# Performance work log

Measured on AMD Instinct MI355X. Metric: run time of the kernel, lower is better.

## Reference

```python
import jax, jax.numpy as jnp
import numpy as np
import math

L = 8192          # original_window (signal length)
WIN = 128         # config.small_window == n_features
STRIDE = 32       # config.small_stride
EMB = 128         # embedding_dim -> rnn2 hidden
HID = 2 * EMB     # rnn1 hidden
B = 256


def _window_starts(length, w, s):
    count = math.ceil((length - w) / s)
    starts = [i * s for i in range(count)]
    if count * s < length:
        starts.append(length - w)  # trailing window, mirrors torch code
    return np.asarray(starts, dtype=np.int32)


def sliding_window(x):
    starts = _window_starts(L, WIN, STRIDE)          # [T]
    idx = starts[:, None] + np.arange(WIN)[None, :]
    return x[:, idx]


def lstm(x, W_ih, W_hh, b_ih, b_hh):
    # x: [B, T, I]; torch gate order i, f, g, o. Returns (all h: [B,T,H], last h: [B,H])
    H = W_hh.shape[1]
    bsz = x.shape[0]
    xg = jnp.einsum('bti,gi->btg', x, W_ih) + b_ih + b_hh  # precompute input gates [B,T,4H]

    def step(carry, g):
        h, c = carry
        g = g + h @ W_hh.T
        i, f, gg, o = jnp.split(g, 4, axis=-1)
        i = jax.nn.sigmoid(i)
        f = jax.nn.sigmoid(f)
        gg = jnp.tanh(gg)
        o = jax.nn.sigmoid(o)
        c = f * c + i * gg
        h = o * jnp.tanh(c)
        return (h, c), h

    h0 = jnp.zeros((bsz, H), x.dtype)
    c0 = jnp.zeros((bsz, H), x.dtype)
    (h_n, _), hs = jax.lax.scan(step, (h0, c0), jnp.swapaxes(xg, 0, 1))
    return jnp.swapaxes(hs, 0, 1), h_n


def setup_inputs() -> dict:
    key = jax.random.key(0)
    ks = jax.random.split(key, 9)
    s1 = 1.0 / np.sqrt(HID)
    s2 = 1.0 / np.sqrt(EMB)
    return {
        'x': jax.random.normal(ks[0], (B, L), jnp.float32),
        'W_ih1': jax.random.uniform(ks[1], (4 * HID, WIN), jnp.float32, -s1, s1),
        'W_hh1': jax.random.uniform(ks[2], (4 * HID, HID), jnp.float32, -s1, s1),
        'b_ih1': jax.random.uniform(ks[3], (4 * HID,), jnp.float32, -s1, s1),
        'b_hh1': jax.random.uniform(ks[4], (4 * HID,), jnp.float32, -s1, s1),
        'W_ih2': jax.random.uniform(ks[5], (4 * EMB, HID), jnp.float32, -s2, s2),
        'W_hh2': jax.random.uniform(ks[6], (4 * EMB, EMB), jnp.float32, -s2, s2),
        'b_ih2': jax.random.uniform(ks[7], (4 * EMB,), jnp.float32, -s2, s2),
        'b_hh2': jax.random.uniform(ks[8], (4 * EMB,), jnp.float32, -s2, s2),
    }


def reference(x, W_ih1, W_hh1, b_ih1, b_hh1, W_ih2, W_hh2, b_ih2, b_hh2):
    xw = sliding_window(x)
    h1, _ = lstm(xw, W_ih1, W_hh1, b_ih1, b_hh1)  # [B, T, HID]
    _, h_n = lstm(h1, W_ih2, W_hh2, b_ih2, b_hh2)  # [B, EMB]
    return h_n.reshape((x.shape[0], EMB))
```

## Files before the change

### kernel.cpp

```cpp
#include <hip/hip_runtime.h>
#include <stdint.h>

#define L_SIG   8192
#define T_STEPS 253
#define H1      256
#define H2      128
#define NBATCH  256

typedef __attribute__((ext_vector_type(8))) short short8;
typedef __attribute__((ext_vector_type(4))) float f32x4;
typedef unsigned int uint32x4 __attribute__((ext_vector_type(4)));
typedef unsigned int uint32x2 __attribute__((ext_vector_type(2)));

__device__ __forceinline__ ushort f2bf(float f){
  uint32_t u = __builtin_bit_cast(uint32_t, f);
  u += 0x7FFFu + ((u >> 16) & 1u);
  return (ushort)(u >> 16);
}
__device__ __forceinline__ float bf2f(ushort h){
  uint32_t u = ((uint32_t)h) << 16;
  return __builtin_bit_cast(float, u);
}
__device__ __forceinline__ float sigm(float x){ return 1.0f / (1.0f + __expf(-x)); }
__device__ __forceinline__ float tanhfast(float x){ return 1.0f - 2.0f / (__expf(2.0f*x) + 1.0f); }
__device__ __forceinline__ int swz(int u){ return u ^ ((u >> 3) & 7); }
__device__ __forceinline__ void load_coh(uint32x4& r, const unsigned int* p){
  asm volatile("global_load_dwordx4 %0, %1, off sc0 sc1" : "=&v"(r) : "v"(p));
}

__global__ __launch_bounds__(256, 1)
void encoder_kernel(const float* __restrict__ x,
                    const float* __restrict__ Wih1, const float* __restrict__ Whh1,
                    const float* __restrict__ bih1, const float* __restrict__ bhh1,
                    const float* __restrict__ Wih2, const float* __restrict__ Whh2,
                    const float* __restrict__ bih2, const float* __restrict__ bhh2,
                    float* __restrict__ out,
                    unsigned int* sync_ws,
                    unsigned int* h1buf,
                    unsigned int* h2buf)
{
  __shared__ ushort sh_hi[16][520];
  __shared__ ushort sh_lo[16][520];
  __shared__ float  sC1[4][16][20];
  __shared__ float  sC2[2][2][16][20];

  const int tid  = threadIdx.x;
  const int lane = tid & 63;
  const int wv   = tid >> 6;
  const int bid  = blockIdx.x;
  const int grp = 2 * (bid & 7) + (bid >> 7);
  const int bi  = (bid & 127) >> 3;
  const int B0  = grp * 16;
  const int D1  = bi * 16;
  const int D2  = bi * 8;

  short8 B1h[12], B1l[12];
  short8 B2h[6],  B2l[6];
  {
    const int nn = lane & 15, p = lane >> 4;
    const int R1 = wv * 256 + D1 + nn;
    #pragma unroll
    for (int kk = 0; kk < 12; ++kk){
      short8 h8, l8;
      #pragma unroll
      for (int j = 0; j < 8; ++j){
        const int k = 32*kk + 8*p + j;
        const float v = (k < 128) ? Wih1[R1*128 + k] : Whh1[R1*256 + (k - 128)];
        const ushort hb = f2bf(v);
        h8[j] = (short)hb;
        l8[j] = (short)f2bf(v - bf2f(hb));
      }
      B1h[kk] = h8; B1l[kk] = l8;
    }
    const int tw = wv & 1, kh = wv >> 1;
    const int rr = tw*16 + nn;
    const int R2 = (rr >> 3) * 128 + D2 + (rr & 7);
    #pragma unroll
    for (int i = 0; i < 6; ++i){
      const int kk2 = 6*kh + i;
      short8 h8, l8;
      #pragma unroll
      for (int j = 0; j < 8; ++j){
        const int k = 32*kk2 + 8*p + j;
        const float v = (k < 256) ? Wih2[R2*256 + k] : Whh2[R2*128 + (k - 256)];
        const ushort hb = f2bf(v);
        h8[j] = (short)hb;
        l8[j] = (short)f2bf(v - bf2f(hb));
      }
      B2h[i] = h8; B2l[i] = l8;
    }
  }

  const int eb  = tid >> 4, ed  = tid & 15;
  const int eb2 = (tid & 127) >> 3, ed2 = tid & 7;
  float bs1[4], bs2[4];
  #pragma unroll
  for (int g = 0; g < 4; ++g){
    bs1[g] = bih1[g*256 + D1 + ed]  + bhh1[g*256 + D1 + ed];
    bs2[g] = bih2[g*128 + D2 + ed2] + bhh2[g*128 + D2 + ed2];
  }

  float c1 = 0.f, c2 = 0.f;
  unsigned int* slots = sync_ws + grp * 64;

  auto stageX = [&](int wn){
    const int bx = tid >> 4, cx = tid & 15;
    const float* xp = x + (size_t)(B0 + bx) * L_SIG + 32*wn + 8*cx;
    const float4 v0 = *(const float4*)xp;
    const float4 v1 = *(const float4*)(xp + 4);
    float f[8] = {v0.x, v0.y, v0.z, v0.w, v1.x, v1.y, v1.z, v1.w};
    union { ushort s[8]; uint32x4 v; } H, L;
    #pragma unroll
    for (int j = 0; j < 8; ++j){
      const ushort hb = f2bf(f[j]);
      H.s[j] = hb;
      L.s[j] = f2bf(f[j] - bf2f(hb));
    }
    const int u = swz(cx);
    *(uint32x4*)&sh_hi[bx][8*u] = H.v;
    *(uint32x4*)&sh_lo[bx][8*u] = L.v;
  };

  auto wrState = [&](uint32x4 q, int b, int us){
    union { ushort s[4]; uint32x2 v; } Hh, Ll;
    #pragma unroll
    for (int k = 0; k < 4; ++k){
      const unsigned int u = q[k];
      Hh.s[k] = (ushort)(u & 0xFFFFu);
      Ll.s[k] = (ushort)(u >> 16);
    }
    *(uint32x2*)&sh_hi[b][us] = Hh.v;
    *(uint32x2*)&sh_lo[b][us] = Ll.v;
  };

  auto stageState = [&](int n){
    const unsigned int* h1p = h1buf + (size_t)(n & 1)*(NBATCH*H1) + (size_t)B0*H1 + 4*tid;
    uint32x4 q0, q1, q2, q3, q4, q5;
    load_coh(q0, h1p);
    load_coh(q1, h1p + 1024);
    load_coh(q2, h1p + 2048);
    load_coh(q3, h1p + 3072);
    const bool h2v = (n >= 1);
    if (h2v){
      const unsigned int* h2p = h2buf + (size_t)((n-1) & 1)*(NBATCH*H2) + (size_t)B0*H2 + 4*tid;
      load_coh(q4, h2p);
      load_coh(q5, h2p + 1024);
    }
    asm volatile("s_waitcnt vmcnt(0)" ::: "memory");
    __builtin_amdgcn_sched_barrier(0);
    {
      const int t6 = tid & 63;
      const int us = 8*swz(16 + (t6 >> 1)) + 4*(t6 & 1);
      const int b0r = tid >> 6;
      wrState(q0, b0r + 0,  us);
      wrState(q1, b0r + 4,  us);
      wrState(q2, b0r + 8,  us);
      wrState(q3, b0r + 12, us);
    }
    {
      const int t5 = tid & 31;
      const int us = 8*swz(48 + (t5 >> 1)) + 4*(t5 & 1);
      const int b0r = tid >> 5;
      if (h2v){
        wrState(q4, b0r + 0, us);
        wrState(q5, b0r + 8, us);
      } else {
        uint32x2 z = {0, 0};
        *(uint32x2*)&sh_hi[b0r + 0][us] = z; *(uint32x2*)&sh_lo[b0r + 0][us] = z;
        *(uint32x2*)&sh_hi[b0r + 8][us] = z; *(uint32x2*)&sh_lo[b0r + 8][us] = z;
      }
    }
  };

  for (int i = tid; i < 16*384; i += 256){
    const int b = i / 384, c = 128 + (i % 384);
    const int us = 8*swz(c >> 3) + (c & 7);
    sh_hi[b][us] = 0; sh_lo[b][us] = 0;
  }
  stageX(0);
  __syncthreads();

  for (int n = 0; n <= T_STEPS; ++n){
    const int m = lane & 15, p = lane >> 4;
    if (n < T_STEPS){
      f32x4 hh = {0,0,0,0}, hl = {0,0,0,0}, lh = {0,0,0,0};
      #pragma unroll
      for (int kk = 0; kk < 12; ++kk){
        const int u = swz(4*kk + p);
        const short8 ah = *(const short8*)&sh_hi[m][8*u];
        const short8 al = *(const short8*)&sh_lo[m][8*u];
        hh = __builtin_amdgcn_mfma_f32_16x16x32_bf16(ah, B1h[kk], hh, 0, 0, 0);
        hl = __builtin_amdgcn_mfma_f32_16x16x32_bf16(ah, B1l[kk], hl, 0, 0, 0);
        lh = __builtin_amdgcn_mfma_f32_16x16x32_bf16(al, B1h[kk], lh, 0, 0, 0);
      }
      const f32x4 cs = hh + hl + lh;
      #pragma unroll
      for (int r = 0; r < 4; ++r) sC1[wv][4*p + r][m] = cs[r];
    }
    if (n >= 1){
      const int tw = wv & 1, kh = wv >> 1;
      f32x4 hh = {0,0,0,0}, hl = {0,0,0,0}, lh = {0,0,0,0};
      #pragma unroll
      for (int i = 0; i < 6; ++i){
        const int u = swz(16 + 4*(6*kh + i) + p);
        const short8 ah = *(const short8*)&sh_hi[m][8*u];
        const short8 al = *(const short8*)&sh_lo[m][8*u];
        hh = __builtin_amdgcn_mfma_f32_16x16x32_bf16(ah, B2h[i], hh, 0, 0, 0);
        hl = __builtin_amdgcn_mfma_f32_16x16x32_bf16(ah, B2l[i], hl, 0, 0, 0);
        lh = __builtin_amdgcn_mfma_f32_16x16x32_bf16(al, B2h[i], lh, 0, 0, 0);
      }
      const f32x4 cs = hh + hl + lh;
      #pragma unroll
      for (int r = 0; r < 4; ++r) sC2[tw][kh][4*p + r][m] = cs[r];
    }
    __syncthreads();

    if (n < T_STEPS){
      float gi = sC1[0][eb][ed] + bs1[0];
      float gf = sC1[1][eb][ed] + bs1[1];
      float gg = sC1[2][eb][ed] + bs1[2];
      float go = sC1[3][eb][ed] + bs1[3];
      c1 = sigm(gf)*c1 + sigm(gi)*tanhfast(gg);
      const float h = sigm(go)*tanhfast(c1);
      const ushort hb = f2bf(h);
      const ushort lb = f2bf(h - bf2f(hb));
      __hip_atomic_store(
          &h1buf[(size_t)(n & 1)*(NBATCH*H1) + (size_t)(B0 + eb)*H1 + D1 + ed],
          (uint32_t)hb | ((uint32_t)lb << 16),
          __ATOMIC_RELAXED, __HIP_MEMORY_SCOPE_AGENT);
    }
    if (n >= 1 && tid < 128){
      float gi = sC2[0][0][eb2][ed2]   + sC2[0][1][eb2][ed2]   + bs2[0];
      float gf = sC2[0][0][eb2][8+ed2] + sC2[0][1][eb2][8+ed2] + bs2[1];
      float gg = sC2[1][0][eb2][ed2]   + sC2[1][1][eb2][ed2]   + bs2[2];
      float go = sC2[1][0][eb2][8+ed2] + sC2[1][1][eb2][8+ed2] + bs2[3];
      c2 = sigm(gf)*c2 + sigm(gi)*tanhfast(gg);
      const float h = sigm(go)*tanhfast(c2);
      if (n == T_STEPS){
        out[(size_t)(B0 + eb2)*H2 + D2 + ed2] = h;
      } else {
        const ushort hb = f2bf(h);
        const ushort lb = f2bf(h - bf2f(hb));
        __hip_atomic_store(
            &h2buf[(size_t)((n-1) & 1)*(NBATCH*H2) + (size_t)(B0 + eb2)*H2 + D2 + ed2],
            (uint32_t)hb | ((uint32_t)lb << 16),
            __ATOMIC_RELAXED, __HIP_MEMORY_SCOPE_AGENT);
      }
    }

    if (n < T_STEPS){
      __syncthreads();
      if (tid == 0){
        __hip_atomic_store(&slots[bi], (unsigned int)(n + 1),
                           __ATOMIC_RELAXED, __HIP_MEMORY_SCOPE_AGENT);
      }
      if (n + 1 < T_STEPS) stageX(n + 1);
      if (wv == 0){
        const unsigned int tgt = (unsigned int)(n + 1);
        while (true){
          const unsigned int v = __hip_atomic_load(&slots[lane & 15],
                                                   __ATOMIC_RELAXED, __HIP_MEMORY_SCOPE_AGENT);
          if (__all(v >= tgt)) break;
          __builtin_amdgcn_s_sleep(1);
        }
      }
      __syncthreads();
      stageState(n);
      __syncthreads();
    }
  }
}

extern "C" void kernel_launch(void* const* d_in, const int* in_sizes, int n_in,
                              void* d_out, int out_size, void* d_ws, size_t ws_size,
                              hipStream_t stream)
{
  const float* x    = (const float*)d_in[0];
  const float* Wih1 = (const float*)d_in[1];
  const float* Whh1 = (const float*)d_in[2];
  const float* bih1 = (const float*)d_in[3];
  const float* bhh1 = (const float*)d_in[4];
  const float* Wih2 = (const float*)d_in[5];
  const float* Whh2 = (const float*)d_in[6];
  const float* bih2 = (const float*)d_in[7];
  const float* bhh2 = (const float*)d_in[8];

  uint8_t*      ws    = (uint8_t*)d_ws;
  unsigned int* syncp = (unsigned int*)ws;
  unsigned int* h1buf = (unsigned int*)(ws + 4096);
  unsigned int* h2buf = (unsigned int*)(ws + 4096 + 2*NBATCH*H1*4);

  hipMemsetAsync(syncp, 0, 4096, stream);
  encoder_kernel<<<dim3(256), dim3(256), 0, stream>>>(
      x, Wih1, Whh1, bih1, bhh1, Wih2, Whh2, bih2, bhh2,
      (float*)d_out, syncp, h1buf, h2buf);
}
```

Measured before the change: 759.7 us.

## Replace flag barrier with step-tagged state words and split K across waves

Each hidden-state word now carries its step counter in a 64-bit pair, so consumers poll the state data directly instead of a separate per-block slot array. This removes a block barrier, the flag store and the spin loop per step. The MFMA work is also reorganised so each wave takes a K-slice for all gates, with partial sums reduced through shared memory, and the hl/lh accumulators are merged. In exchange, each state read is twice as wide, every thread re-polls a dozen vector loads until all tags match, and the host memset is larger.

```diff
diff --git a/kernel.cpp b/kernel.cpp
--- a/kernel.cpp
+++ b/kernel.cpp
@@ -24,8 +24,11 @@
 __device__ __forceinline__ float sigm(float x){ return 1.0f / (1.0f + __expf(-x)); }
 __device__ __forceinline__ float tanhfast(float x){ return 1.0f - 2.0f / (__expf(2.0f*x) + 1.0f); }
 __device__ __forceinline__ int swz(int u){ return u ^ ((u >> 3) & 7); }
-__device__ __forceinline__ void load_coh(uint32x4& r, const unsigned int* p){
+__device__ __forceinline__ void load4(uint32x4& r, const unsigned int* p){
   asm volatile("global_load_dwordx4 %0, %1, off sc0 sc1" : "=&v"(r) : "v"(p));
+}
+__device__ __forceinline__ void store2_coh(unsigned int* p, uint32x2 v){
+  asm volatile("global_store_dwordx2 %0, %1, off sc0 sc1" :: "v"(p), "v"(v) : "memory");
 }
 
 __global__ __launch_bounds__(256, 1)
@@ -35,14 +38,13 @@
                     const float* __restrict__ Wih2, const float* __restrict__ Whh2,
                     const float* __restrict__ bih2, const float* __restrict__ bhh2,
                     float* __restrict__ out,
-                    unsigned int* sync_ws,
-                    unsigned int* h1buf,
-                    unsigned int* h2buf)
+                    unsigned long long* h1t,
+                    unsigned long long* h2t)
 {
   __shared__ ushort sh_hi[16][520];
   __shared__ ushort sh_lo[16][520];
-  __shared__ float  sC1[4][16][20];
-  __shared__ float  sC2[2][2][16][20];
+  __shared__ float  sC1[4][4][16][20];
+  __shared__ float  sC2[4][2][16][20];
 
   const int tid  = threadIdx.x;
   const int lane = tid & 63;
@@ -58,36 +60,40 @@
   short8 B2h[6],  B2l[6];
   {
     const int nn = lane & 15, p = lane >> 4;
-    const int R1 = wv * 256 + D1 + nn;
     #pragma unroll
-    for (int kk = 0; kk < 12; ++kk){
-      short8 h8, l8;
-      #pragma unroll
-      for (int j = 0; j < 8; ++j){
-        const int k = 32*kk + 8*p + j;
-        const float v = (k < 128) ? Wih1[R1*128 + k] : Whh1[R1*256 + (k - 128)];
-        const ushort hb = f2bf(v);
-        h8[j] = (short)hb;
-        l8[j] = (short)f2bf(v - bf2f(hb));
-      }
-      B1h[kk] = h8; B1l[kk] = l8;
-    }
-    const int tw = wv & 1, kh = wv >> 1;
-    const int rr = tw*16 + nn;
-    const int R2 = (rr >> 3) * 128 + D2 + (rr & 7);
+    for (int g = 0; g < 4; ++g){
+      const int R1 = g * 256 + D1 + nn;
+      #pragma unroll
+      for (int i = 0; i < 3; ++i){
+        short8 h8, l8;
+        #pragma unroll
+        for (int j = 0; j < 8; ++j){
+          const int k = 32*(3*wv + i) + 8*p + j;
+          const float v = (k < 128) ? Wih1[R1*128 + k] : Whh1[R1*256 + (k - 128)];
+          const ushort hb = f2bf(v);
+          h8[j] = (short)hb;
+          l8[j] = (short)f2bf(v - bf2f(hb));
+        }
+        B1h[g*3 + i] = h8; B1l[g*3 + i] = l8;
+      }
+    }
     #pragma unroll
-    for (int i = 0; i < 6; ++i){
-      const int kk2 = 6*kh + i;
-      short8 h8, l8;
-      #pragma unroll
-      for (int j = 0; j < 8; ++j){
-        const int k = 32*kk2 + 8*p + j;
-        const float v = (k < 256) ? Wih2[R2*256 + k] : Whh2[R2*128 + (k - 256)];
-        const ushort hb = f2bf(v);
-        h8[j] = (short)hb;
-        l8[j] = (short)f2bf(v - bf2f(hb));
-      }
-      B2h[i] = h8; B2l[i] = l8;
+    for (int tw = 0; tw < 2; ++tw){
+      const int rr = tw*16 + nn;
+      const int R2 = (rr >> 3) * 128 + D2 + (rr & 7);
+      #pragma unroll
+      for (int i = 0; i < 3; ++i){
+        short8 h8, l8;
+        #pragma unroll
+        for (int j = 0; j < 8; ++j){
+          const int k = 32*(3*wv + i) + 8*p + j;
+          const float v = (k < 256) ? Wih2[R2*256 + k] : Whh2[R2*128 + (k - 256)];
+          const ushort hb = f2bf(v);
+          h8[j] = (short)hb;
+          l8[j] = (short)f2bf(v - bf2f(hb));
+        }
+        B2h[tw*3 + i] = h8; B2l[tw*3 + i] = l8;
+      }
     }
   }
 
@@ -101,7 +107,6 @@
   }
 
   float c1 = 0.f, c2 = 0.f;
-  unsigned int* slots = sync_ws + grp * 64;
 
   auto stageX = [&](int wn){
     const int bx = tid >> 4, cx = tid & 15;
@@ -121,119 +126,85 @@
     *(uint32x4*)&sh_lo[bx][8*u] = L.v;
   };
 
-  auto wrState = [&](uint32x4 q, int b, int us){
-    union { ushort s[4]; uint32x2 v; } Hh, Ll;
-    #pragma unroll
-    for (int k = 0; k < 4; ++k){
-      const unsigned int u = q[k];
-      Hh.s[k] = (ushort)(u & 0xFFFFu);
-      Ll.s[k] = (ushort)(u >> 16);
-    }
-    *(uint32x2*)&sh_hi[b][us] = Hh.v;
-    *(uint32x2*)&sh_lo[b][us] = Ll.v;
-  };
-
-  auto stageState = [&](int n){
-    const unsigned int* h1p = h1buf + (size_t)(n & 1)*(NBATCH*H1) + (size_t)B0*H1 + 4*tid;
-    uint32x4 q0, q1, q2, q3, q4, q5;
-    load_coh(q0, h1p);
-    load_coh(q1, h1p + 1024);
-    load_coh(q2, h1p + 2048);
-    load_coh(q3, h1p + 3072);
-    const bool h2v = (n >= 1);
-    if (h2v){
-      const unsigned int* h2p = h2buf + (size_t)((n-1) & 1)*(NBATCH*H2) + (size_t)B0*H2 + 4*tid;
-      load_coh(q4, h2p);
-      load_coh(q5, h2p + 1024);
-    }
-    asm volatile("s_waitcnt vmcnt(0)" ::: "memory");
-    __builtin_amdgcn_sched_barrier(0);
-    {
-      const int t6 = tid & 63;
-      const int us = 8*swz(16 + (t6 >> 1)) + 4*(t6 & 1);
-      const int b0r = tid >> 6;
-      wrState(q0, b0r + 0,  us);
-      wrState(q1, b0r + 4,  us);
-      wrState(q2, b0r + 8,  us);
-      wrState(q3, b0r + 12, us);
-    }
-    {
-      const int t5 = tid & 31;
-      const int us = 8*swz(48 + (t5 >> 1)) + 4*(t5 & 1);
-      const int b0r = tid >> 5;
-      if (h2v){
-        wrState(q4, b0r + 0, us);
-        wrState(q5, b0r + 8, us);
-      } else {
-        uint32x2 z = {0, 0};
-        *(uint32x2*)&sh_hi[b0r + 0][us] = z; *(uint32x2*)&sh_lo[b0r + 0][us] = z;
-        *(uint32x2*)&sh_hi[b0r + 8][us] = z; *(uint32x2*)&sh_lo[b0r + 8][us] = z;
-      }
-    }
-  };
-
-  for (int i = tid; i < 16*384; i += 256){
-    const int b = i / 384, c = 128 + (i % 384);
-    const int us = 8*swz(c >> 3) + (c & 7);
-    sh_hi[b][us] = 0; sh_lo[b][us] = 0;
+  {
+    uint32x4 z = {0,0,0,0};
+    for (int i = tid; i < 16*48; i += 256){
+      const int b = i / 48, u = 16 + (i % 48);
+      *(uint32x4*)&sh_hi[b][8*swz(u)] = z;
+      *(uint32x4*)&sh_lo[b][8*swz(u)] = z;
+    }
   }
   stageX(0);
   __syncthreads();
 
+  const int m = lane & 15, p = lane >> 4;
+
   for (int n = 0; n <= T_STEPS; ++n){
-    const int m = lane & 15, p = lane >> 4;
     if (n < T_STEPS){
-      f32x4 hh = {0,0,0,0}, hl = {0,0,0,0}, lh = {0,0,0,0};
-      #pragma unroll
-      for (int kk = 0; kk < 12; ++kk){
-        const int u = swz(4*kk + p);
+      f32x4 aH[4] = {{0,0,0,0},{0,0,0,0},{0,0,0,0},{0,0,0,0}};
+      f32x4 aM[4] = {{0,0,0,0},{0,0,0,0},{0,0,0,0},{0,0,0,0}};
+      #pragma unroll
+      for (int i = 0; i < 3; ++i){
+        const int u = swz(4*(3*wv + i) + p);
         const short8 ah = *(const short8*)&sh_hi[m][8*u];
         const short8 al = *(const short8*)&sh_lo[m][8*u];
-        hh = __builtin_amdgcn_mfma_f32_16x16x32_bf16(ah, B1h[kk], hh, 0, 0, 0);
-        hl = __builtin_amdgcn_mfma_f32_16x16x32_bf16(ah, B1l[kk], hl, 0, 0, 0);
-        lh = __builtin_amdgcn_mfma_f32_16x16x32_bf16(al, B1h[kk], lh, 0, 0, 0);
-      }
-      const f32x4 cs = hh + hl + lh;
-      #pragma unroll
-      for (int r = 0; r < 4; ++r) sC1[wv][4*p + r][m] = cs[r];
+        #pragma unroll
+        for (int g = 0; g < 4; ++g){
+          aH[g] = __builtin_amdgcn_mfma_f32_16x16x32_bf16(ah, B1h[g*3+i], aH[g], 0, 0, 0);
+          aM[g] = __builtin_amdgcn_mfma_f32_16x16x32_bf16(ah, B1l[g*3+i], aM[g], 0, 0, 0);
+          aM[g] = __builtin_amdgcn_mfma_f32_16x16x32_bf16(al, B1h[g*3+i], aM[g], 0, 0, 0);
+        }
+      }
+      #pragma unroll
+      for (int g = 0; g < 4; ++g){
+        const f32x4 cs = aH[g] + aM[g];
+        *(f32x4*)&sC1[wv][g][m][4*p] = cs;
+      }
     }
     if (n >= 1){
-      const int tw = wv & 1, kh = wv >> 1;
-      f32x4 hh = {0,0,0,0}, hl = {0,0,0,0}, lh = {0,0,0,0};
-      #pragma unroll
-      for (int i = 0; i < 6; ++i){
-        const int u = swz(16 + 4*(6*kh + i) + p);
+      f32x4 aH[2] = {{0,0,0,0},{0,0,0,0}};
+      f32x4 aM[2] = {{0,0,0,0},{0,0,0,0}};
+      #pragma unroll
+      for (int i = 0; i < 3; ++i){
+        const int u = swz(16 + 4*(3*wv + i) + p);
         const short8 ah = *(const short8*)&sh_hi[m][8*u];
         const short8 al = *(const short8*)&sh_lo[m][8*u];
-        hh = __builtin_amdgcn_mfma_f32_16x16x32_bf16(ah, B2h[i], hh, 0, 0, 0);
-        hl = __builtin_amdgcn_mfma_f32_16x16x32_bf16(ah, B2l[i], hl, 0, 0, 0);
-        lh = __builtin_amdgcn_mfma_f32_16x16x32_bf16(al, B2h[i], lh, 0, 0, 0);
-      }
-      const f32x4 cs = hh + hl + lh;
-      #pragma unroll
-      for (int r = 0; r < 4; ++r) sC2[tw][kh][4*p + r][m] = cs[r];
+        #pragma unroll
+        for (int tw = 0; tw < 2; ++tw){
+          aH[tw] = __builtin_amdgcn_mfma_f32_16x16x32_bf16(ah, B2h[tw*3+i], aH[tw], 0, 0, 0);
+          aM[tw] = __builtin_amdgcn_mfma_f32_16x16x32_bf16(ah, B2l[tw*3+i], aM[tw], 0, 0, 0);
+          aM[tw] = __builtin_amdgcn_mfma_f32_16x16x32_bf16(al, B2h[tw*3+i], aM[tw], 0, 0, 0);
+        }
+      }
+      #pragma unroll
+      for (int tw = 0; tw < 2; ++tw){
+        const f32x4 cs = aH[tw] + aM[tw];
+        *(f32x4*)&sC2[wv][tw][m][4*p] = cs;
+      }
     }
     __syncthreads();
 
     if (n < T_STEPS){
-      float gi = sC1[0][eb][ed] + bs1[0];
-      float gf = sC1[1][eb][ed] + bs1[1];
-      float gg = sC1[2][eb][ed] + bs1[2];
-      float go = sC1[3][eb][ed] + bs1[3];
-      c1 = sigm(gf)*c1 + sigm(gi)*tanhfast(gg);
-      const float h = sigm(go)*tanhfast(c1);
+      float gv[4];
+      #pragma unroll
+      for (int g = 0; g < 4; ++g)
+        gv[g] = sC1[0][g][ed][eb] + sC1[1][g][ed][eb]
+              + sC1[2][g][ed][eb] + sC1[3][g][ed][eb] + bs1[g];
+      c1 = sigm(gv[1])*c1 + sigm(gv[0])*tanhfast(gv[2]);
+      const float h = sigm(gv[3])*tanhfast(c1);
       const ushort hb = f2bf(h);
       const ushort lb = f2bf(h - bf2f(hb));
-      __hip_atomic_store(
-          &h1buf[(size_t)(n & 1)*(NBATCH*H1) + (size_t)(B0 + eb)*H1 + D1 + ed],
-          (uint32_t)hb | ((uint32_t)lb << 16),
-          __ATOMIC_RELAXED, __HIP_MEMORY_SCOPE_AGENT);
+      uint32x2 pv;
+      pv[0] = (uint32_t)hb | ((uint32_t)lb << 16);
+      pv[1] = (unsigned)(n + 1);
+      store2_coh((unsigned int*)(h1t + (size_t)(n & 1)*(NBATCH*H1)
+                                 + (size_t)(B0 + eb)*H1 + D1 + ed), pv);
     }
     if (n >= 1 && tid < 128){
-      float gi = sC2[0][0][eb2][ed2]   + sC2[0][1][eb2][ed2]   + bs2[0];
-      float gf = sC2[0][0][eb2][8+ed2] + sC2[0][1][eb2][8+ed2] + bs2[1];
-      float gg = sC2[1][0][eb2][ed2]   + sC2[1][1][eb2][ed2]   + bs2[2];
-      float go = sC2[1][0][eb2][8+ed2] + sC2[1][1][eb2][8+ed2] + bs2[3];
+      float gi = sC2[0][0][ed2][eb2]   + sC2[1][0][ed2][eb2]   + sC2[2][0][ed2][eb2]   + sC2[3][0][ed2][eb2]   + bs2[0];
+      float gf = sC2[0][0][8+ed2][eb2] + sC2[1][0][8+ed2][eb2] + sC2[2][0][8+ed2][eb2] + sC2[3][0][8+ed2][eb2] + bs2[1];
+      float gg = sC2[0][1][ed2][eb2]   + sC2[1][1][ed2][eb2]   + sC2[2][1][ed2][eb2]   + sC2[3][1][ed2][eb2]   + bs2[2];
+      float go = sC2[0][1][8+ed2][eb2] + sC2[1][1][8+ed2][eb2] + sC2[2][1][8+ed2][eb2] + sC2[3][1][8+ed2][eb2] + bs2[3];
       c2 = sigm(gf)*c2 + sigm(gi)*tanhfast(gg);
       const float h = sigm(go)*tanhfast(c2);
       if (n == T_STEPS){
@@ -241,31 +212,66 @@
       } else {
         const ushort hb = f2bf(h);
         const ushort lb = f2bf(h - bf2f(hb));
-        __hip_atomic_store(
-            &h2buf[(size_t)((n-1) & 1)*(NBATCH*H2) + (size_t)(B0 + eb2)*H2 + D2 + ed2],
-            (uint32_t)hb | ((uint32_t)lb << 16),
-            __ATOMIC_RELAXED, __HIP_MEMORY_SCOPE_AGENT);
+        uint32x2 pv;
+        pv[0] = (uint32_t)hb | ((uint32_t)lb << 16);
+        pv[1] = (unsigned)n;
+        store2_coh((unsigned int*)(h2t + (size_t)((n-1) & 1)*(NBATCH*H2)
+                                   + (size_t)(B0 + eb2)*H2 + D2 + ed2), pv);
       }
     }
 
     if (n < T_STEPS){
-      __syncthreads();
-      if (tid == 0){
-        __hip_atomic_store(&slots[bi], (unsigned int)(n + 1),
-                           __ATOMIC_RELAXED, __HIP_MEMORY_SCOPE_AGENT);
-      }
+      const unsigned int* q1 = (const unsigned int*)h1t
+          + (size_t)(n & 1)*(2*NBATCH*H1) + (size_t)B0*(2*H1) + 4*tid;
+      const unsigned int* q2 = (const unsigned int*)h2t
+          + (size_t)((n - 1) & 1)*(2*NBATCH*H2) + (size_t)B0*(2*H2) + 4*tid;
+      uint32x4 a[8], c[4];
+      #pragma unroll
+      for (int j = 0; j < 8; ++j) load4(a[j], q1 + 1024*j);
+      #pragma unroll
+      for (int j = 0; j < 4; ++j) load4(c[j], q2 + 1024*j);
       if (n + 1 < T_STEPS) stageX(n + 1);
-      if (wv == 0){
-        const unsigned int tgt = (unsigned int)(n + 1);
-        while (true){
-          const unsigned int v = __hip_atomic_load(&slots[lane & 15],
-                                                   __ATOMIC_RELAXED, __HIP_MEMORY_SCOPE_AGENT);
-          if (__all(v >= tgt)) break;
-          __builtin_amdgcn_s_sleep(1);
-        }
-      }
-      __syncthreads();
-      stageState(n);
+      asm volatile("s_waitcnt vmcnt(0)" ::: "memory");
+      __builtin_amdgcn_sched_barrier(0);
+      const unsigned et1 = (unsigned)(n + 1), et2 = (unsigned)n;
+      bool ok = true;
+      #pragma unroll
+      for (int j = 0; j < 8; ++j) ok = ok && (a[j][1] >= et1) && (a[j][3] >= et1);
+      #pragma unroll
+      for (int j = 0; j < 4; ++j) ok = ok && (c[j][1] >= et2) && (c[j][3] >= et2);
+      while (!ok){
+        #pragma unroll
+        for (int j = 0; j < 8; ++j) load4(a[j], q1 + 1024*j);
+        #pragma unroll
+        for (int j = 0; j < 4; ++j) load4(c[j], q2 + 1024*j);
+        asm volatile("s_waitcnt vmcnt(0)" ::: "memory");
+        __builtin_amdgcn_sched_barrier(0);
+        ok = true;
+        #pragma unroll
+        for (int j = 0; j < 8; ++j) ok = ok && (a[j][1] >= et1) && (a[j][3] >= et1);
+        #pragma unroll
+        for (int j = 0; j < 4; ++j) ok = ok && (c[j][1] >= et2) && (c[j][3] >= et2);
+      }
+      {
+        const int th = tid >> 7;
+        const int d0 = (2*tid) & 255;
+        const int off1 = 8*swz(16 + (d0 >> 3)) + (d0 & 7);
+        #pragma unroll
+        for (int j = 0; j < 8; ++j){
+          const uint32_t v0 = a[j][0], v1 = a[j][2];
+          *(uint32_t*)&sh_hi[2*j + th][off1] = (v0 & 0xFFFFu) | (v1 << 16);
+          *(uint32_t*)&sh_lo[2*j + th][off1] = (v0 >> 16) | (v1 & 0xFFFF0000u);
+        }
+        const int t6 = (tid >> 6) & 3;
+        const int d2 = (2*tid) & 127;
+        const int off2 = 8*swz(48 + (d2 >> 3)) + (d2 & 7);
+        #pragma unroll
+        for (int j = 0; j < 4; ++j){
+          const uint32_t v0 = c[j][0], v1 = c[j][2];
+          *(uint32_t*)&sh_hi[4*j + t6][off2] = (v0 & 0xFFFFu) | (v1 << 16);
+          *(uint32_t*)&sh_lo[4*j + t6][off2] = (v0 >> 16) | (v1 & 0xFFFF0000u);
+        }
+      }
       __syncthreads();
     }
   }
@@ -285,13 +291,12 @@
   const float* bih2 = (const float*)d_in[7];
   const float* bhh2 = (const float*)d_in[8];
 
-  uint8_t*      ws    = (uint8_t*)d_ws;
-  unsigned int* syncp = (unsigned int*)ws;
-  unsigned int* h1buf = (unsigned int*)(ws + 4096);
-  unsigned int* h2buf = (unsigned int*)(ws + 4096 + 2*NBATCH*H1*4);
-
-  hipMemsetAsync(syncp, 0, 4096, stream);
+  uint8_t* ws = (uint8_t*)d_ws;
+  unsigned long long* h1t = (unsigned long long*)ws;
+  unsigned long long* h2t = (unsigned long long*)(ws + (1u << 20));
+
+  hipMemsetAsync(ws, 0, (1u << 20) + (512u << 10), stream);
   encoder_kernel<<<dim3(256), dim3(256), 0, stream>>>(
       x, Wih1, Whh1, bih1, bhh1, Wih2, Whh2, bih2, bhh2,
-      (float*)d_out, syncp, h1buf, h2buf);
-}
+      (float*)d_out, h1t, h2t);
+}
```

Result: slower. 1.459 ms (+92.0%).
